# Performance work log

Measured on AMD Instinct MI355X. Metric: run time of the kernel, lower is better.

Reference implementation:

```python
import jax, jax.numpy as jnp
import numpy as np

N_NODES = 50000
N_EDGES = 600000
H = 128


def setup_inputs() -> dict:
    key = jax.random.key(0)
    ks = jax.random.split(key, 7)
    node_emb = jax.random.normal(ks[0], (N_NODES, H), dtype=jnp.float32)
    # PyTorch Linear default init ~ U(-1/sqrt(fan_in), 1/sqrt(fan_in)); scaled normal is fine for a baseline
    W1 = jax.random.normal(ks[1], (H, 2 * H), dtype=jnp.float32) * (1.0 / np.sqrt(2 * H))
    b1 = jax.random.normal(ks[2], (H,), dtype=jnp.float32) * 0.01
    W2 = jax.random.normal(ks[3], (1, H), dtype=jnp.float32) * (1.0 / np.sqrt(H))
    b2 = jax.random.normal(ks[4], (1,), dtype=jnp.float32) * 0.01
    src = jax.random.randint(ks[5], (N_EDGES,), 0, N_NODES, dtype=jnp.int64)
    dst = jax.random.randint(ks[6], (N_EDGES,), 0, N_NODES, dtype=jnp.int64)
    return {"node_emb": node_emb, "W1": W1, "b1": b1, "W2": W2, "b2": b2,
            "src": src, "dst": dst}


def reference(node_emb, W1, b1, W2, b2, src, dst):
    # gather per-edge endpoint embeddings and concat -> [E, 2H]
    h = jnp.concatenate([node_emb[src], node_emb[dst]], axis=1)
    # 2-layer MLP: Linear(2H->H) -> ReLU -> Linear(H->1) -> squeeze
    hidden = jax.nn.relu(h @ W1.T + b1)          # [E, H]
    scores = hidden @ W2.T + b2                   # [E, 1]
    return scores[:, 0]                           # [E]
```

## Files before the change

kernel.cpp:

```cpp
#include <hip/hip_runtime.h>
#include <hip/hip_bf16.h>


#define H   128
#define NJJ 256
#define BM  32
#define EPW 32

typedef __attribute__((ext_vector_type(8))) short  frag_ab;
typedef __attribute__((ext_vector_type(4))) float  f32x4;
typedef __attribute__((ext_vector_type(4))) unsigned int   uint4v;
typedef __attribute__((ext_vector_type(2))) unsigned int   uint2v;

__device__ __forceinline__ unsigned short f2bf(float x) {
    unsigned int u = __float_as_uint(x);
    unsigned int r = u + 0x7FFFu + ((u >> 16) & 1u);
    return (unsigned short)(r >> 16);
}

__device__ __forceinline__ unsigned int pk_bf16(float lo, float hi) {
    unsigned int r;
    asm("v_cvt_pk_bf16_f32 %0, %1, %2" : "=v"(r) : "v"(lo), "v"(hi));
    return r;
}

__device__ __forceinline__ frag_ab relu_sum(uint4v s, uint4v d) {
    uint4v r;
#pragma unroll
    for (int p = 0; p < 4; ++p) {
        float sl = __uint_as_float(s[p] << 16);
        float sh = __uint_as_float(s[p] & 0xFFFF0000u);
        float dl = __uint_as_float(d[p] << 16);
        float dh = __uint_as_float(d[p] & 0xFFFF0000u);
        float l = sl + dl; l = l > 0.f ? l : 0.f;
        float h = sh + dh; h = h > 0.f ? h : 0.f;
        r[p] = pk_bf16(l, h);
    }
    return __builtin_bit_cast(frag_ab, r);
}

__global__ __launch_bounds__(256)
void convert_weights(const float* __restrict__ W1, const float* __restrict__ W2,
                     unsigned short* __restrict__ W1f, unsigned short* __restrict__ W2c) {
    if (blockIdx.x == 128) {
        int j = threadIdx.x;
        if (j < H) {
            int pos = (j >> 6) * 64 + 4 * (j & 15) + ((j & 63) >> 4);
            W2c[pos] = f2bf(W2[j]);
        }
        return;
    }
    int idx = blockIdx.x * 256 + threadIdx.x;
    int e     = idx & 7;
    int chunk = idx >> 3;
    int lane  = chunk & 63;
    int ks    = (chunk >> 6) & 3;
    int cf    = (chunk >> 8) & 3;
    int wid   = chunk >> 10;
    int col   = wid * 64 + (lane & 15) + cf * 16;
    int k     = ks * 32 + (lane >> 4) * 8 + e;
    W1f[idx] = f2bf(W1[(size_t)(col & 127) * 256 + (size_t)(col >> 7) * H + k]);
}

__device__ __forceinline__ int swz_chunk(int c, int row) {
    return (c & ~7) | ((c ^ row) & 7);
}

__global__ __launch_bounds__(256)
void precompute_P_mfma(const float* __restrict__ emb,
                       const unsigned short* __restrict__ W1f,
                       const float* __restrict__ b1,
                       unsigned short* __restrict__ P,
                       int n_nodes) {
    __shared__ __align__(1024) float ldsA[BM * H];
    int tid  = threadIdx.x;
    int lane = tid & 63;
    int wid  = tid >> 6;
    int block0 = blockIdx.x * BM;
    if (block0 + BM > n_nodes) block0 = n_nodes - BM;
    if (block0 < 0) block0 = 0;

    {
#pragma unroll
        for (int j = 0; j < 4; ++j) {
            int row = wid * 8 + j * 2 + (lane >> 5);
            int cp  = lane & 31;
            int c   = swz_chunk(cp, row);
            const float* g = emb + (size_t)(block0 + row) * H + c * 4;
            void* l = (char*)ldsA + wid * 4096 + j * 1024;
            __builtin_amdgcn_global_load_lds(
                (const __attribute__((address_space(1))) void*)g,
                (__attribute__((address_space(3))) void*)l, 16, 0, 0);
        }
    }

    int row16 = lane & 15;
    int g4    = lane >> 4;

    float b1c[4];
#pragma unroll
    for (int cf = 0; cf < 4; ++cf) {
        int col = wid * 64 + cf * 16 + row16;
        b1c[cf] = (col < H) ? b1[col] : 0.f;
    }

    const frag_ab* wf = (const frag_ab*)W1f;
    f32x4 acc[2][4];
#pragma unroll
    for (int mf = 0; mf < 2; ++mf)
#pragma unroll
        for (int cf = 0; cf < 4; ++cf) acc[mf][cf] = (f32x4){0.f, 0.f, 0.f, 0.f};

    frag_ab Bcur[4], Bnxt[4];
#pragma unroll
    for (int cf = 0; cf < 4; ++cf)
        Bcur[cf] = wf[((wid * 4 + cf) * 4 + 0) * 64 + lane];

    __syncthreads();

#pragma unroll 1
    for (int ks = 0; ks < 4; ++ks) {
        if (ks < 3) {
#pragma unroll
            for (int cf = 0; cf < 4; ++cf)
                Bnxt[cf] = wf[((wid * 4 + cf) * 4 + ks + 1) * 64 + lane];
        }
        frag_ab Af[2];
#pragma unroll
        for (int mf = 0; mf < 2; ++mf) {
            int row   = mf * 16 + row16;
            int cbase = ks * 8 + g4 * 2;
            const char* base = (const char*)ldsA + row * 512;
            float4 x = *(const float4*)(base + (swz_chunk(cbase,     row) << 4));
            float4 y = *(const float4*)(base + (swz_chunk(cbase + 1, row) << 4));
            uint4v w;
            w[0] = pk_bf16(x.x, x.y);
            w[1] = pk_bf16(x.z, x.w);
            w[2] = pk_bf16(y.x, y.y);
            w[3] = pk_bf16(y.z, y.w);
            Af[mf] = __builtin_bit_cast(frag_ab, w);
        }
#pragma unroll
        for (int mf = 0; mf < 2; ++mf)
#pragma unroll
            for (int cf = 0; cf < 4; ++cf)
                acc[mf][cf] = __builtin_amdgcn_mfma_f32_16x16x32_bf16(
                    Af[mf], Bcur[cf], acc[mf][cf], 0, 0, 0);
        if (ks < 3) {
#pragma unroll
            for (int cf = 0; cf < 4; ++cf) Bcur[cf] = Bnxt[cf];
        }
    }

#pragma unroll
    for (int mf = 0; mf < 2; ++mf)
#pragma unroll
        for (int r = 0; r < 4; ++r) {
            int row = block0 + mf * 16 + g4 * 4 + r;
            uint2v v;
            v[0] = pk_bf16(acc[mf][0][r] + b1c[0], acc[mf][1][r] + b1c[1]);
            v[1] = pk_bf16(acc[mf][2][r] + b1c[2], acc[mf][3][r] + b1c[3]);
            *(uint2v*)((char*)P + (size_t)row * 512 + wid * 128 + 8 * row16) = v;
        }
}

__global__ __launch_bounds__(256)
void edge_score_mfma(const unsigned short* __restrict__ P,
                     const unsigned short* __restrict__ W2c,
                     const float* __restrict__ b2,
                     const int* __restrict__ src,
                     const int* __restrict__ dst,
                     float* __restrict__ out,
                     int n_edges) {
    int lane = threadIdx.x & 63;
    int wave = blockIdx.x * 4 + (threadIdx.x >> 6);
    int e0 = wave * EPW;
    if (e0 >= n_edges) return;

    frag_ab Bf[4];
    {
        int krun = (lane >> 4) * 8;
#pragma unroll
        for (int ks = 0; ks < 4; ++ks)
            Bf[ks] = *(const frag_ab*)(W2c + ks * 32 + krun);
    }
    float b2v = b2[0];
    int el = lane & 15;
    int kb = (lane >> 4) * 16;

    int eA = e0 + el;       if (eA > n_edges - 1) eA = n_edges - 1;
    int eB = e0 + 16 + el;  if (eB > n_edges - 1) eB = n_edges - 1;
    const char* pb = (const char*)P;
    const char* sA = pb + (size_t)src[eA] * 512 + kb;
    const char* dA = pb + (size_t)dst[eA] * 512 + 256 + kb;
    const char* sB = pb + (size_t)src[eB] * 512 + kb;
    const char* dB = pb + (size_t)dst[eB] * 512 + 256 + kb;

    uint4v rsA[4], rdA[4], rsB[4], rdB[4];
#pragma unroll
    for (int ks = 0; ks < 4; ++ks) {
        rsA[ks] = *(const uint4v*)(sA + ks * 64);
        rdA[ks] = *(const uint4v*)(dA + ks * 64);
        rsB[ks] = *(const uint4v*)(sB + ks * 64);
        rdB[ks] = *(const uint4v*)(dB + ks * 64);
    }

    f32x4 accA = (f32x4){0.f, 0.f, 0.f, 0.f};
    f32x4 accB = (f32x4){0.f, 0.f, 0.f, 0.f};
#pragma unroll
    for (int ks = 0; ks < 4; ++ks) {
        accA = __builtin_amdgcn_mfma_f32_16x16x32_bf16(relu_sum(rsA[ks], rdA[ks]), Bf[ks], accA, 0, 0, 0);
        accB = __builtin_amdgcn_mfma_f32_16x16x32_bf16(relu_sum(rsB[ks], rdB[ks]), Bf[ks], accB, 0, 0, 0);
    }

    if (el == 0) {
        int r0 = (lane >> 4) * 4;
        int ea = e0 + r0, eb = e0 + 16 + r0;
        float4 oA = { accA[0] + b2v, accA[1] + b2v, accA[2] + b2v, accA[3] + b2v };
        float4 oB = { accB[0] + b2v, accB[1] + b2v, accB[2] + b2v, accB[3] + b2v };
        if (eb + 3 < n_edges) {
            *(float4*)(out + ea) = oA;
            *(float4*)(out + eb) = oB;
        } else {
#pragma unroll
            for (int r = 0; r < 4; ++r) {
                if (ea + r < n_edges) out[ea + r] = accA[r] + b2v;
                if (eb + r < n_edges) out[eb + r] = accB[r] + b2v;
            }
        }
    }
}

__global__ __launch_bounds__(128)
void naive_edge(const float* __restrict__ emb,
                const float* __restrict__ W1,
                const float* __restrict__ b1,
                const float* __restrict__ W2,
                const float* __restrict__ b2,
                const int* __restrict__ src,
                const int* __restrict__ dst,
                float* __restrict__ out,
                int n_edges) {
    __shared__ float es[H], ed[H];
    __shared__ float red[2];
    int e = blockIdx.x;
    if (e >= n_edges) return;
    int j = threadIdx.x;
    int s = src[e], d = dst[e];
    es[j] = emb[(size_t)s * H + j];
    ed[j] = emb[(size_t)d * H + j];
    __syncthreads();
    const float* w = W1 + (size_t)j * 256;
    float acc = b1[j];
    for (int k = 0; k < H; ++k) acc += es[k] * w[k] + ed[k] * w[H + k];
    acc = acc > 0.f ? acc : 0.f;
    float p = acc * W2[j];
#pragma unroll
    for (int off = 32; off; off >>= 1) p += __shfl_xor(p, off, 64);
    int lane = j & 63, wid = j >> 6;
    if (lane == 0) red[wid] = p;
    __syncthreads();
    if (j == 0) out[e] = red[0] + red[1] + b2[0];
}

extern "C" void kernel_launch(void* const* d_in, const int* in_sizes, int n_in,
                              void* d_out, int out_size, void* d_ws, size_t ws_size,
                              hipStream_t stream) {
    const float* emb = (const float*)d_in[0];
    const float* W1  = (const float*)d_in[1];
    const float* b1  = (const float*)d_in[2];
    const float* W2  = (const float*)d_in[3];
    const float* b2  = (const float*)d_in[4];
    const int*   src = (const int*)d_in[5];
    const int*   dst = (const int*)d_in[6];
    float* out = (float*)d_out;

    int n_nodes = in_sizes[0] / H;
    int n_edges = in_sizes[5];

    size_t needP = (size_t)n_nodes * NJJ * sizeof(unsigned short);
    size_t offW1 = (needP + 255) & ~(size_t)255;
    size_t offW2 = offW1 + (size_t)NJJ * H * sizeof(unsigned short);
    size_t need  = offW2 + 256;

    if (ws_size >= need && n_nodes >= BM) {
        unsigned short* P   = (unsigned short*)d_ws;
        unsigned short* W1f = (unsigned short*)((char*)d_ws + offW1);
        unsigned short* W2c = (unsigned short*)((char*)d_ws + offW2);
        convert_weights<<<129, 256, 0, stream>>>(W1, W2, W1f, W2c);
        int grid1 = (n_nodes + BM - 1) / BM;
        precompute_P_mfma<<<grid1, 256, 0, stream>>>(emb, W1f, b1, P, n_nodes);
        int grid2 = (n_edges + EPW * 4 - 1) / (EPW * 4);
        edge_score_mfma<<<grid2, 256, 0, stream>>>(P, W2c, b2, src, dst, out, n_edges);
    } else {
        naive_edge<<<n_edges, 128, 0, stream>>>(emb, W1, b1, W2, b2, src, dst, out, n_edges);
    }
}
```

Baseline: 64.50 us.

## Fuse weight conversion, node projection and edge scoring into one cooperative persistent kernel

Merges the three launches (weight conversion, per-node projection, per-edge scoring) into a single persistent kernel launched cooperatively, with grid-wide barriers between phases and grid-stride loops over node tiles and edge groups. The aim is to remove the launch gaps and tail effects between the separate kernels. In exchange it adds two grid.sync barriers, host-side occupancy queries on every call, and persistent loops that may lower per-phase parallelism and occupancy.

Measured after the change: 239.7 us. 272% more time.

```diff
diff --git a/kernel.cpp b/kernel.cpp
--- a/kernel.cpp
+++ b/kernel.cpp
@@ -1,5 +1,7 @@
 #include <hip/hip_runtime.h>
 #include <hip/hip_bf16.h>
+#include <hip/hip_cooperative_groups.h>
+namespace cg = cooperative_groups;
 
 
 #define H   128
@@ -39,48 +41,67 @@
     return __builtin_bit_cast(frag_ab, r);
 }
 
-__global__ __launch_bounds__(256)
-void convert_weights(const float* __restrict__ W1, const float* __restrict__ W2,
-                     unsigned short* __restrict__ W1f, unsigned short* __restrict__ W2c) {
-    if (blockIdx.x == 128) {
-        int j = threadIdx.x;
-        if (j < H) {
-            int pos = (j >> 6) * 64 + 4 * (j & 15) + ((j & 63) >> 4);
-            W2c[pos] = f2bf(W2[j]);
-        }
-        return;
-    }
-    int idx = blockIdx.x * 256 + threadIdx.x;
-    int e     = idx & 7;
-    int chunk = idx >> 3;
-    int lane  = chunk & 63;
-    int ks    = (chunk >> 6) & 3;
-    int cf    = (chunk >> 8) & 3;
-    int wid   = chunk >> 10;
-    int col   = wid * 64 + (lane & 15) + cf * 16;
-    int k     = ks * 32 + (lane >> 4) * 8 + e;
-    W1f[idx] = f2bf(W1[(size_t)(col & 127) * 256 + (size_t)(col >> 7) * H + k]);
-}
-
 __device__ __forceinline__ int swz_chunk(int c, int row) {
     return (c & ~7) | ((c ^ row) & 7);
 }
 
-__global__ __launch_bounds__(256)
-void precompute_P_mfma(const float* __restrict__ emb,
-                       const unsigned short* __restrict__ W1f,
-                       const float* __restrict__ b1,
-                       unsigned short* __restrict__ P,
-                       int n_nodes) {
+__global__ __launch_bounds__(256, 4)
+void fused_mlp(const float* __restrict__ emb,
+               const float* __restrict__ W1,
+               const float* __restrict__ b1,
+               const float* __restrict__ W2,
+               const float* __restrict__ b2,
+               const int* __restrict__ src,
+               const int* __restrict__ dst,
+               unsigned short* __restrict__ W1f,
+               unsigned short* __restrict__ W2c,
+               unsigned short* __restrict__ P,
+               float* __restrict__ out,
+               int n_nodes, int n_edges, int nblocks) {
+    cg::grid_group grid = cg::this_grid();
     __shared__ __align__(1024) float ldsA[BM * H];
+
     int tid  = threadIdx.x;
     int lane = tid & 63;
     int wid  = tid >> 6;
-    int block0 = blockIdx.x * BM;
-    if (block0 + BM > n_nodes) block0 = n_nodes - BM;
-    if (block0 < 0) block0 = 0;
-
-    {
+    int bid  = blockIdx.x;
+    int row16 = lane & 15;
+    int g4    = lane >> 4;
+
+    for (int gidx = bid * 256 + tid; gidx < 32768 + H; gidx += nblocks * 256) {
+        if (gidx < 32768) {
+            int e     = gidx & 7;
+            int chunk = gidx >> 3;
+            int l2    = chunk & 63;
+            int ks    = (chunk >> 6) & 3;
+            int cf    = (chunk >> 8) & 3;
+            int w2    = chunk >> 10;
+            int col   = w2 * 64 + (l2 & 15) + cf * 16;
+            int k     = ks * 32 + (l2 >> 4) * 8 + e;
+            W1f[gidx] = f2bf(W1[(size_t)(col & 127) * 256 + (size_t)(col >> 7) * H + k]);
+        } else {
+            int j = gidx - 32768;
+            int pos = (j >> 6) * 64 + 4 * (j & 15) + ((j & 63) >> 4);
+            W2c[pos] = f2bf(W2[j]);
+        }
+    }
+    __threadfence();
+    grid.sync();
+
+    const frag_ab* wf = (const frag_ab*)W1f;
+    float b1c[4];
+#pragma unroll
+    for (int cf = 0; cf < 4; ++cf) {
+        int col = wid * 64 + cf * 16 + row16;
+        b1c[cf] = (col < H) ? b1[col] : 0.f;
+    }
+
+    int ntiles = (n_nodes + BM - 1) / BM;
+    for (int t = bid; t < ntiles; t += nblocks) {
+        int block0 = t * BM;
+        if (block0 + BM > n_nodes) block0 = n_nodes - BM;
+        if (block0 < 0) block0 = 0;
+
 #pragma unroll
         for (int j = 0; j < 4; ++j) {
             int row = wid * 8 + j * 2 + (lane >> 5);
@@ -92,140 +113,122 @@
                 (const __attribute__((address_space(1))) void*)g,
                 (__attribute__((address_space(3))) void*)l, 16, 0, 0);
         }
-    }
-
-    int row16 = lane & 15;
-    int g4    = lane >> 4;
-
-    float b1c[4];
-#pragma unroll
-    for (int cf = 0; cf < 4; ++cf) {
-        int col = wid * 64 + cf * 16 + row16;
-        b1c[cf] = (col < H) ? b1[col] : 0.f;
-    }
-
-    const frag_ab* wf = (const frag_ab*)W1f;
-    f32x4 acc[2][4];
-#pragma unroll
-    for (int mf = 0; mf < 2; ++mf)
-#pragma unroll
-        for (int cf = 0; cf < 4; ++cf) acc[mf][cf] = (f32x4){0.f, 0.f, 0.f, 0.f};
-
-    frag_ab Bcur[4], Bnxt[4];
-#pragma unroll
-    for (int cf = 0; cf < 4; ++cf)
-        Bcur[cf] = wf[((wid * 4 + cf) * 4 + 0) * 64 + lane];
-
-    __syncthreads();
+
+        f32x4 acc[2][4];
+#pragma unroll
+        for (int mf = 0; mf < 2; ++mf)
+#pragma unroll
+            for (int cf = 0; cf < 4; ++cf) acc[mf][cf] = (f32x4){0.f, 0.f, 0.f, 0.f};
+
+        frag_ab Bcur[4], Bnxt[4];
+#pragma unroll
+        for (int cf = 0; cf < 4; ++cf)
+            Bcur[cf] = wf[((wid * 4 + cf) * 4 + 0) * 64 + lane];
+
+        __syncthreads();
 
 #pragma unroll 1
-    for (int ks = 0; ks < 4; ++ks) {
-        if (ks < 3) {
-#pragma unroll
-            for (int cf = 0; cf < 4; ++cf)
-                Bnxt[cf] = wf[((wid * 4 + cf) * 4 + ks + 1) * 64 + lane];
-        }
-        frag_ab Af[2];
-#pragma unroll
-        for (int mf = 0; mf < 2; ++mf) {
-            int row   = mf * 16 + row16;
-            int cbase = ks * 8 + g4 * 2;
-            const char* base = (const char*)ldsA + row * 512;
-            float4 x = *(const float4*)(base + (swz_chunk(cbase,     row) << 4));
-            float4 y = *(const float4*)(base + (swz_chunk(cbase + 1, row) << 4));
-            uint4v w;
-            w[0] = pk_bf16(x.x, x.y);
-            w[1] = pk_bf16(x.z, x.w);
-            w[2] = pk_bf16(y.x, y.y);
-            w[3] = pk_bf16(y.z, y.w);
-            Af[mf] = __builtin_bit_cast(frag_ab, w);
-        }
+        for (int ks = 0; ks < 4; ++ks) {
+            if (ks < 3) {
+#pragma unroll
+                for (int cf = 0; cf < 4; ++cf)
+                    Bnxt[cf] = wf[((wid * 4 + cf) * 4 + ks + 1) * 64 + lane];
+            }
+            frag_ab Af[2];
+#pragma unroll
+            for (int mf = 0; mf < 2; ++mf) {
+                int row   = mf * 16 + row16;
+                int cbase = ks * 8 + g4 * 2;
+                const char* base = (const char*)ldsA + row * 512;
+                float4 x = *(const float4*)(base + (swz_chunk(cbase,     row) << 4));
+                float4 y = *(const float4*)(base + (swz_chunk(cbase + 1, row) << 4));
+                uint4v w;
+                w[0] = pk_bf16(x.x, x.y);
+                w[1] = pk_bf16(x.z, x.w);
+                w[2] = pk_bf16(y.x, y.y);
+                w[3] = pk_bf16(y.z, y.w);
+                Af[mf] = __builtin_bit_cast(frag_ab, w);
+            }
+#pragma unroll
+            for (int mf = 0; mf < 2; ++mf)
+#pragma unroll
+                for (int cf = 0; cf < 4; ++cf)
+                    acc[mf][cf] = __builtin_amdgcn_mfma_f32_16x16x32_bf16(
+                        Af[mf], Bcur[cf], acc[mf][cf], 0, 0, 0);
+            if (ks < 3) {
+#pragma unroll
+                for (int cf = 0; cf < 4; ++cf) Bcur[cf] = Bnxt[cf];
+            }
+        }
+        __syncthreads();
+
 #pragma unroll
         for (int mf = 0; mf < 2; ++mf)
 #pragma unroll
-            for (int cf = 0; cf < 4; ++cf)
-                acc[mf][cf] = __builtin_amdgcn_mfma_f32_16x16x32_bf16(
-                    Af[mf], Bcur[cf], acc[mf][cf], 0, 0, 0);
-        if (ks < 3) {
-#pragma unroll
-            for (int cf = 0; cf < 4; ++cf) Bcur[cf] = Bnxt[cf];
-        }
-    }
-
-#pragma unroll
-    for (int mf = 0; mf < 2; ++mf)
-#pragma unroll
-        for (int r = 0; r < 4; ++r) {
-            int row = block0 + mf * 16 + g4 * 4 + r;
-            uint2v v;
-            v[0] = pk_bf16(acc[mf][0][r] + b1c[0], acc[mf][1][r] + b1c[1]);
-            v[1] = pk_bf16(acc[mf][2][r] + b1c[2], acc[mf][3][r] + b1c[3]);
-            *(uint2v*)((char*)P + (size_t)row * 512 + wid * 128 + 8 * row16) = v;
-        }
-}
-
-__global__ __launch_bounds__(256)
-void edge_score_mfma(const unsigned short* __restrict__ P,
-                     const unsigned short* __restrict__ W2c,
-                     const float* __restrict__ b2,
-                     const int* __restrict__ src,
-                     const int* __restrict__ dst,
-                     float* __restrict__ out,
-                     int n_edges) {
-    int lane = threadIdx.x & 63;
-    int wave = blockIdx.x * 4 + (threadIdx.x >> 6);
-    int e0 = wave * EPW;
-    if (e0 >= n_edges) return;
+            for (int r = 0; r < 4; ++r) {
+                int row = block0 + mf * 16 + g4 * 4 + r;
+                uint2v v;
+                v[0] = pk_bf16(acc[mf][0][r] + b1c[0], acc[mf][1][r] + b1c[1]);
+                v[1] = pk_bf16(acc[mf][2][r] + b1c[2], acc[mf][3][r] + b1c[3]);
+                *(uint2v*)((char*)P + (size_t)row * 512 + wid * 128 + 8 * row16) = v;
+            }
+    }
+    __threadfence();
+    grid.sync();
 
     frag_ab Bf[4];
     {
-        int krun = (lane >> 4) * 8;
+        int krun = g4 * 8;
 #pragma unroll
         for (int ks = 0; ks < 4; ++ks)
             Bf[ks] = *(const frag_ab*)(W2c + ks * 32 + krun);
     }
     float b2v = b2[0];
-    int el = lane & 15;
-    int kb = (lane >> 4) * 16;
-
-    int eA = e0 + el;       if (eA > n_edges - 1) eA = n_edges - 1;
-    int eB = e0 + 16 + el;  if (eB > n_edges - 1) eB = n_edges - 1;
-    const char* pb = (const char*)P;
-    const char* sA = pb + (size_t)src[eA] * 512 + kb;
-    const char* dA = pb + (size_t)dst[eA] * 512 + 256 + kb;
-    const char* sB = pb + (size_t)src[eB] * 512 + kb;
-    const char* dB = pb + (size_t)dst[eB] * 512 + 256 + kb;
-
-    uint4v rsA[4], rdA[4], rsB[4], rdB[4];
-#pragma unroll
-    for (int ks = 0; ks < 4; ++ks) {
-        rsA[ks] = *(const uint4v*)(sA + ks * 64);
-        rdA[ks] = *(const uint4v*)(dA + ks * 64);
-        rsB[ks] = *(const uint4v*)(sB + ks * 64);
-        rdB[ks] = *(const uint4v*)(dB + ks * 64);
-    }
-
-    f32x4 accA = (f32x4){0.f, 0.f, 0.f, 0.f};
-    f32x4 accB = (f32x4){0.f, 0.f, 0.f, 0.f};
-#pragma unroll
-    for (int ks = 0; ks < 4; ++ks) {
-        accA = __builtin_amdgcn_mfma_f32_16x16x32_bf16(relu_sum(rsA[ks], rdA[ks]), Bf[ks], accA, 0, 0, 0);
-        accB = __builtin_amdgcn_mfma_f32_16x16x32_bf16(relu_sum(rsB[ks], rdB[ks]), Bf[ks], accB, 0, 0, 0);
-    }
-
-    if (el == 0) {
-        int r0 = (lane >> 4) * 4;
-        int ea = e0 + r0, eb = e0 + 16 + r0;
-        float4 oA = { accA[0] + b2v, accA[1] + b2v, accA[2] + b2v, accA[3] + b2v };
-        float4 oB = { accB[0] + b2v, accB[1] + b2v, accB[2] + b2v, accB[3] + b2v };
-        if (eb + 3 < n_edges) {
-            *(float4*)(out + ea) = oA;
-            *(float4*)(out + eb) = oB;
-        } else {
-#pragma unroll
-            for (int r = 0; r < 4; ++r) {
-                if (ea + r < n_edges) out[ea + r] = accA[r] + b2v;
-                if (eb + r < n_edges) out[eb + r] = accB[r] + b2v;
+    int el = row16;
+    int kb = g4 * 16;
+    int ngroups = (n_edges + EPW - 1) / EPW;
+
+    for (int grp = bid * 4 + wid; grp < ngroups; grp += nblocks * 4) {
+        int e0 = grp * EPW;
+        int eA = e0 + el;       if (eA > n_edges - 1) eA = n_edges - 1;
+        int eB = e0 + 16 + el;  if (eB > n_edges - 1) eB = n_edges - 1;
+        const char* pb = (const char*)P;
+        const char* sA = pb + (size_t)src[eA] * 512 + kb;
+        const char* dA = pb + (size_t)dst[eA] * 512 + 256 + kb;
+        const char* sB = pb + (size_t)src[eB] * 512 + kb;
+        const char* dB = pb + (size_t)dst[eB] * 512 + 256 + kb;
+
+        uint4v rsA[4], rdA[4], rsB[4], rdB[4];
+#pragma unroll
+        for (int ks = 0; ks < 4; ++ks) {
+            rsA[ks] = *(const uint4v*)(sA + ks * 64);
+            rdA[ks] = *(const uint4v*)(dA + ks * 64);
+            rsB[ks] = *(const uint4v*)(sB + ks * 64);
+            rdB[ks] = *(const uint4v*)(dB + ks * 64);
+        }
+
+        f32x4 accA = (f32x4){0.f, 0.f, 0.f, 0.f};
+        f32x4 accB = (f32x4){0.f, 0.f, 0.f, 0.f};
+#pragma unroll
+        for (int ks = 0; ks < 4; ++ks) {
+            accA = __builtin_amdgcn_mfma_f32_16x16x32_bf16(relu_sum(rsA[ks], rdA[ks]), Bf[ks], accA, 0, 0, 0);
+            accB = __builtin_amdgcn_mfma_f32_16x16x32_bf16(relu_sum(rsB[ks], rdB[ks]), Bf[ks], accB, 0, 0, 0);
+        }
+
+        if (el == 0) {
+            int r0 = g4 * 4;
+            int ea = e0 + r0, eb = e0 + 16 + r0;
+            float4 oA = { accA[0] + b2v, accA[1] + b2v, accA[2] + b2v, accA[3] + b2v };
+            float4 oB = { accB[0] + b2v, accB[1] + b2v, accB[2] + b2v, accB[3] + b2v };
+            if (eb + 3 < n_edges) {
+                *(float4*)(out + ea) = oA;
+                *(float4*)(out + eb) = oB;
+            } else {
+#pragma unroll
+                for (int r = 0; r < 4; ++r) {
+                    if (ea + r < n_edges) out[ea + r] = accA[r] + b2v;
+                    if (eb + r < n_edges) out[eb + r] = accB[r] + b2v;
+                }
             }
         }
     }
@@ -283,15 +286,22 @@
     size_t offW2 = offW1 + (size_t)NJJ * H * sizeof(unsigned short);
     size_t need  = offW2 + 256;
 
-    if (ws_size >= need && n_nodes >= BM) {
+    int cu = 256, maxBlk = 0;
+    hipDeviceGetAttribute(&cu, hipDeviceAttributeMultiprocessorCount, 0);
+    hipOccupancyMaxActiveBlocksPerMultiprocessor(&maxBlk, (const void*)fused_mlp, 256, 0);
+    int nblocks = cu * (maxBlk > 0 ? maxBlk : 1);
+    if (nblocks > 2048) nblocks = 2048;
+
+    if (ws_size >= need && n_nodes >= BM && maxBlk >= 1) {
         unsigned short* P   = (unsigned short*)d_ws;
         unsigned short* W1f = (unsigned short*)((char*)d_ws + offW1);
         unsigned short* W2c = (unsigned short*)((char*)d_ws + offW2);
-        convert_weights<<<129, 256, 0, stream>>>(W1, W2, W1f, W2c);
-        int grid1 = (n_nodes + BM - 1) / BM;
-        precompute_P_mfma<<<grid1, 256, 0, stream>>>(emb, W1f, b1, P, n_nodes);
-        int grid2 = (n_edges + EPW * 4 - 1) / (EPW * 4);
-        edge_score_mfma<<<grid2, 256, 0, stream>>>(P, W2c, b2, src, dst, out, n_edges);
+        void* args[] = { (void*)&emb, (void*)&W1, (void*)&b1, (void*)&W2, (void*)&b2,
+                         (void*)&src, (void*)&dst, (void*)&W1f, (void*)&W2c,
+                         (void*)&P, (void*)&out, (void*)&n_nodes, (void*)&n_edges,
+                         (void*)&nblocks };
+        hipLaunchCooperativeKernel((const void*)fused_mlp, dim3(nblocks), dim3(256),
+                                   args, 0, stream);
     } else {
         naive_edge<<<n_edges, 128, 0, stream>>>(emb, W1, b1, W2, b2, src, dst, out, n_edges);
     }
```
